# Kernel optimization log

Measured on AMD Instinct MI355X. Metric: run time of the kernel, lower is better.

Reference implementation:

```python
import jax, jax.numpy as jnp
import numpy as np

B, S, C, H, L = 8, 1000, 512, 8, 6
D = C // H  # 64


def setup_inputs() -> dict:
    key = jax.random.key(0)
    ks = jax.random.split(key, 6)
    s = 0.02
    x = jax.random.normal(ks[0], (B, S, C), dtype=jnp.float32)
    ln_g = jnp.ones((L, C), jnp.float32)
    ln_b = jnp.zeros((L, C), jnp.float32)
    Wq = jax.random.normal(ks[1], (L, C, C), jnp.float32) * s
    Wk = jax.random.normal(ks[2], (L, C, C), jnp.float32) * s
    Wv = jax.random.normal(ks[3], (L, C, C), jnp.float32) * s
    Wo = jax.random.normal(ks[4], (L, C, C), jnp.float32) * s
    bq = jnp.zeros((L, C), jnp.float32)
    bk = jnp.zeros((L, C), jnp.float32)
    bv = jnp.zeros((L, C), jnp.float32)
    bo = jnp.zeros((L, C), jnp.float32)
    return dict(x=x, ln_g=ln_g, ln_b=ln_b, Wq=Wq, bq=bq, Wk=Wk, bk=bk,
                Wv=Wv, bv=bv, Wo=Wo, bo=bo)


def _layer_norm(x, g, b, eps=1e-5):
    m = jnp.mean(x, axis=-1, keepdims=True)
    v = jnp.mean(jnp.square(x - m), axis=-1, keepdims=True)
    return (x - m) * jax.lax.rsqrt(v + eps) * g + b


def reference(x, ln_g, ln_b, Wq, bq, Wk, bk, Wv, bv, Wo, bo):
    # First streaming call: history is empty, so q = k = v = x for every
    # layer (x is never updated between layers); only the last layer's
    # output is returned. Mask is all-ones (no-op); dropout is eval-mode.
    Bn, Sn, Cn = x.shape
    scale = 1.0 / np.sqrt(D).astype(np.float32)
    # additive relative-position bias: pos[i, j] = i - j
    pos = (jnp.arange(Sn)[:, None] - jnp.arange(Sn)[None, :]).astype(x.dtype)
    out = x
    for i in range(L):
        xn = _layer_norm(x, ln_g[i], ln_b[i])  # same LN for q, k, v
        q = (xn @ Wq[i].T + bq[i]).reshape(Bn, Sn, H, D)
        k = (xn @ Wk[i].T + bk[i]).reshape(Bn, Sn, H, D)
        v = (xn @ Wv[i].T + bv[i]).reshape(Bn, Sn, H, D)
        scores = jnp.einsum('bqhd,bkhd->bhqk', q, k) * scale + pos  # [B,H,S,S]
        attn = jax.nn.softmax(scores, axis=-1)
        ctx = jnp.einsum('bhqk,bkhd->bqhd', attn, v).reshape(Bn, Sn, Cn)
        out = ctx @ Wo[i].T + bo[i]
    return out
```

## Files before the change

### kernel.cpp

```cpp
#include <hip/hip_runtime.h>
#include <math.h>


typedef __bf16 bf16x8 __attribute__((ext_vector_type(8)));
typedef __bf16 bf16x4 __attribute__((ext_vector_type(4)));
typedef float f32x4 __attribute__((ext_vector_type(4)));

__device__ __forceinline__ void async16(const __bf16* g, __bf16* l) {
  __builtin_amdgcn_global_load_lds((const __attribute__((address_space(1))) void*)g,
                                   (__attribute__((address_space(3))) void*)l, 16, 0, 0);
}

__global__ __launch_bounds__(256) void prep_k(const float* __restrict__ Wq, const float* __restrict__ Wk,
                                              const float* __restrict__ Wv, const float* __restrict__ Wo,
                                              __bf16* __restrict__ wdst,
                                              const float* __restrict__ x, const float* __restrict__ lg,
                                              const float* __restrict__ lb, __bf16* __restrict__ y) {
  const int bid = blockIdx.x;
  if (bid < 1024) {
    const float* src = (bid < 256) ? Wq : (bid < 512) ? Wk : (bid < 768) ? Wv : Wo;
    int idx = ((bid & 255) * 256 + threadIdx.x) * 4;
    float4 v = *(const float4*)(src + idx);
    bf16x4 o = {(__bf16)v.x, (__bf16)v.y, (__bf16)v.z, (__bf16)v.w};
    *(bf16x4*)(wdst + (size_t)(bid >> 8) * 262144 + idx) = o;
    return;
  }
  const int row = (bid - 1024) * 4 + (threadIdx.x >> 6);
  const int l = threadIdx.x & 63;
  const float* xr = x + (size_t)row * 512 + l * 8;
  float4 a = *(const float4*)xr, c = *(const float4*)(xr + 4);
  float s = a.x + a.y + a.z + a.w + c.x + c.y + c.z + c.w;
#pragma unroll
  for (int m = 1; m < 64; m <<= 1) s += __shfl_xor(s, m, 64);
  float mean = s * (1.0f / 512.0f);
  float d[8] = {a.x - mean, a.y - mean, a.z - mean, a.w - mean,
                c.x - mean, c.y - mean, c.z - mean, c.w - mean};
  float qq = 0.f;
#pragma unroll
  for (int e = 0; e < 8; ++e) qq += d[e] * d[e];
#pragma unroll
  for (int m = 1; m < 64; m <<= 1) qq += __shfl_xor(qq, m, 64);
  float rstd = rsqrtf(qq * (1.0f / 512.0f) + 1e-5f);
  float4 g0 = *(const float4*)(lg + l * 8), g1 = *(const float4*)(lg + l * 8 + 4);
  float4 b0 = *(const float4*)(lb + l * 8), b1 = *(const float4*)(lb + l * 8 + 4);
  float gg[8] = {g0.x, g0.y, g0.z, g0.w, g1.x, g1.y, g1.z, g1.w};
  float bb[8] = {b0.x, b0.y, b0.z, b0.w, b1.x, b1.y, b1.z, b1.w};
  bf16x8 o;
#pragma unroll
  for (int e = 0; e < 8; ++e) o[e] = (__bf16)(d[e] * rstd * gg[e] + bb[e]);
  *(bf16x8*)(y + (size_t)row * 512 + l * 8) = o;
}

template <int PROJ>
__global__ __launch_bounds__(256) void gemm_k(const __bf16* __restrict__ A,
                                              const __bf16* __restrict__ Wq_,
                                              const __bf16* __restrict__ Wkv_,
                                              const float* __restrict__ bq_,
                                              const float* __restrict__ bk_,
                                              const float* __restrict__ bv_,
                                              void* __restrict__ Yq_,
                                              __bf16* __restrict__ Ykv_,
                                              int idbase) {
  __shared__ __align__(16) __bf16 Ws[64 * 512];
  const int t = threadIdx.x, w = t >> 6, l = t & 63, g = l >> 4, l15 = l & 15;
  const int id = blockIdx.x + idbase;

  const __bf16* Ab;
  const __bf16* Wt;
  const float* bp;
  int maxrow, ldY;
  void* Yp;
  if (PROJ || id < 512) {
    int low3 = id & 7, rest = id >> 3;
    int n = rest & 7, m = (rest >> 3) * 8 + low3;
    if (m >= 63) return;
    Ab = A + (size_t)m * 128 * 512;
    maxrow = 8000 - m * 128; if (maxrow > 128) maxrow = 128;
    Wt = Wq_ + (size_t)n * 64 * 512;
    bp = bq_ + n * 64;
    ldY = 512;
    Yp = (float*)Yq_ + (size_t)m * 128 * 512 + n * 64;
  } else {
    int kid = id - 512;
    int b = kid & 7, n = kid >> 3;
    Ab = A + (size_t)b * 1000 * 512;
    maxrow = 128;
    Wt = Wkv_ + (size_t)n * 64 * 512;
    int nc = n * 64;
    bp = (nc < 512) ? (bk_ + nc) : (bv_ + (nc - 512));
    ldY = 1024;
    Yp = Ykv_ + (size_t)b * 128 * 1024 + nc;
  }

  float bias_j[4];
#pragma unroll
  for (int j = 0; j < 4; ++j) bias_j[j] = bp[j * 16 + l15];

  int r0 = w * 32 + l15, r1 = r0 + 16;
  int cr0 = (r0 < maxrow) ? r0 : (maxrow - 1);
  int cr1 = (r1 < maxrow) ? r1 : (maxrow - 1);
  const __bf16* a0p = Ab + (size_t)cr0 * 512 + g * 8;
  const __bf16* a1p = Ab + (size_t)cr1 * 512 + g * 8;
  bf16x8 a0 = *(const bf16x8*)a0p;
  bf16x8 a1 = *(const bf16x8*)a1p;

#pragma unroll
  for (int i = 0; i < 16; ++i) {
    int s = i * 256 + t;
    int row = s >> 6, u = s & 63;
    async16(Wt + (size_t)row * 512 + ((u ^ (row & 7)) << 3), &Ws[s * 8]);
  }
  __syncthreads();

  f32x4 acc[2][4] = {};
#pragma unroll
  for (int ks = 0; ks < 16; ++ks) {
    bf16x8 ca0 = a0, ca1 = a1;
    if (ks < 15) {
      a0 = *(const bf16x8*)(a0p + (ks + 1) * 32);
      a1 = *(const bf16x8*)(a1p + (ks + 1) * 32);
    }
    bf16x8 bfr[4];
#pragma unroll
    for (int j = 0; j < 4; ++j) {
      int rb = j * 16 + l15;
      int u = ks * 4 + g;
      bfr[j] = *(const bf16x8*)&Ws[rb * 512 + ((u ^ (rb & 7)) << 3)];
    }
#pragma unroll
    for (int j = 0; j < 4; ++j) {
      acc[0][j] = __builtin_amdgcn_mfma_f32_16x16x32_bf16(ca0, bfr[j], acc[0][j], 0, 0, 0);
      acc[1][j] = __builtin_amdgcn_mfma_f32_16x16x32_bf16(ca1, bfr[j], acc[1][j], 0, 0, 0);
    }
  }

#pragma unroll
  for (int strip = 0; strip < 2; ++strip)
#pragma unroll
    for (int r = 0; r < 4; ++r) {
      int lrow = w * 32 + strip * 16 + g * 4 + r;
      if (lrow < maxrow) {
#pragma unroll
        for (int j = 0; j < 4; ++j) {
          float val = acc[strip][j][r] + bias_j[j];
          if (PROJ) ((float*)Yp)[(size_t)lrow * ldY + j * 16 + l15] = val;
          else      ((__bf16*)Yp)[(size_t)lrow * ldY + j * 16 + l15] = (__bf16)val;
        }
      }
    }
}

__global__ __launch_bounds__(256) void attn_k(const __bf16* __restrict__ xn,
                                              const __bf16* __restrict__ wq,
                                              const float* __restrict__ bq,
                                              const __bf16* __restrict__ kv,
                                              __bf16* __restrict__ ctx) {
  __shared__ __align__(16) __bf16 arena[32768];
  __bf16* Ks = arena;
  __bf16* Vt = arena + 8192;
  __bf16* Qs = arena + 16384;
  __bf16* Ps = arena + 20480;
  const int t = threadIdx.x, w = t >> 6, l = t & 63, g = l >> 4, l15 = l & 15;
  const int id = blockIdx.x;
  const int h = id >> 7, b = (id >> 4) & 7, q0 = (id & 15) * 64;

  const __bf16* Wt = wq + (size_t)h * 64 * 512;
#pragma unroll
  for (int i = 0; i < 16; ++i) {
    int s = i * 256 + t;
    int row = s >> 6, u = s & 63;
    async16(Wt + (size_t)row * 512 + ((u ^ (row & 7)) << 3), &arena[s * 8]);
  }
  int qr = q0 + w * 16 + l15;
  int cqr = (qr > 999) ? 999 : qr;
  const __bf16* a0p = xn + ((size_t)(b * 1000 + cqr)) * 512 + g * 8;
  bf16x8 a0 = *(const bf16x8*)a0p;
  float bias_j[4];
#pragma unroll
  for (int j = 0; j < 4; ++j) bias_j[j] = bq[h * 64 + j * 16 + l15];
  __syncthreads();

  f32x4 acc[4] = {};
#pragma unroll
  for (int ks = 0; ks < 16; ++ks) {
    bf16x8 ca = a0;
    if (ks < 15) a0 = *(const bf16x8*)(a0p + (ks + 1) * 32);
    bf16x8 bfr[4];
#pragma unroll
    for (int j = 0; j < 4; ++j) {
      int rb = j * 16 + l15;
      int u = ks * 4 + g;
      bfr[j] = *(const bf16x8*)&arena[rb * 512 + ((u ^ (rb & 7)) << 3)];
    }
#pragma unroll
    for (int j = 0; j < 4; ++j)
      acc[j] = __builtin_amdgcn_mfma_f32_16x16x32_bf16(ca, bfr[j], acc[j], 0, 0, 0);
  }
  __syncthreads();

#pragma unroll
  for (int i = 0; i < 4; ++i) {
    int s = i * 256 + t;
    int row = s >> 3, u = s & 7;
    async16(kv + (size_t)(b * 128 + row) * 1024 + h * 64 + ((u ^ (row & 7)) << 3), &Ks[s * 8]);
  }
  {
    int vrow = t & 127, dbase = (t >> 7) * 32;
    const __bf16* vp = kv + (size_t)(b * 128 + vrow) * 1024 + 512 + h * 64 + dbase;
#pragma unroll
    for (int c = 0; c < 4; ++c) {
      bf16x8 vv = *(const bf16x8*)(vp + c * 8);
#pragma unroll
      for (int e = 0; e < 8; ++e) {
        int d = dbase + c * 8 + e;
        Vt[d * 128 + (((vrow >> 3) ^ (d & 7)) << 3) + (vrow & 7)] = vv[e];
      }
    }
  }
#pragma unroll
  for (int j = 0; j < 4; ++j)
#pragma unroll
    for (int r = 0; r < 4; ++r) {
      int row = w * 16 + g * 4 + r, col = j * 16 + l15;
      Qs[row * 64 + ((((col >> 3) ^ (row & 7))) << 3) + (col & 7)] =
          (__bf16)(acc[j][r] + bias_j[j]);
    }
  bf16x8 aq[2];
  {
    int row = w * 16 + l15;
    aq[0] = *(const bf16x8*)&Qs[row * 64 + ((g ^ (row & 7)) << 3)];
    aq[1] = *(const bf16x8*)&Qs[row * 64 + (((4 + g) ^ (row & 7)) << 3)];
  }
  __syncthreads();

  f32x4 ct[8] = {};
#pragma unroll
  for (int c = 0; c < 2; ++c)
#pragma unroll
    for (int nt = 0; nt < 8; ++nt) {
      int rn = nt * 16 + l15;
      bf16x8 bkf = *(const bf16x8*)&Ks[rn * 64 + (((c * 4 + g) ^ (rn & 7)) << 3)];
      ct[nt] = __builtin_amdgcn_mfma_f32_16x16x32_bf16(aq[c], bkf, ct[nt], 0, 0, 0);
    }

  __bf16* Pw = Ps + w * 2176;
  float rs[4] = {0.f, 0.f, 0.f, 0.f};
#pragma unroll
  for (int nt = 0; nt < 8; ++nt) {
    int kg = nt * 16 + l15;
#pragma unroll
    for (int r = 0; r < 4; ++r) {
      float p = __expf(ct[nt][r] * 0.125f - (float)kg - 2.0f);
      __bf16 pb = (__bf16)p;
      Pw[(g * 4 + r) * 136 + kg] = pb;
      rs[r] += (float)pb;
    }
  }
#pragma unroll
  for (int r = 0; r < 4; ++r) {
    float s = rs[r];
    s += __shfl_xor(s, 1, 16);
    s += __shfl_xor(s, 2, 16);
    s += __shfl_xor(s, 4, 16);
    s += __shfl_xor(s, 8, 16);
    rs[r] = 1.0f / s;
  }

  f32x4 co[4] = {};
  bf16x8 ap[4];
#pragma unroll
  for (int c = 0; c < 4; ++c) ap[c] = *(const bf16x8*)&Pw[l15 * 136 + c * 32 + g * 8];
#pragma unroll
  for (int nt = 0; nt < 4; ++nt) {
    int d = nt * 16 + l15;
#pragma unroll
    for (int c = 0; c < 4; ++c) {
      bf16x8 bv = *(const bf16x8*)&Vt[d * 128 + (((c * 4 + g) ^ (d & 7)) << 3)];
      co[nt] = __builtin_amdgcn_mfma_f32_16x16x32_bf16(ap[c], bv, co[nt], 0, 0, 0);
    }
  }

#pragma unroll
  for (int r = 0; r < 4; ++r) {
    int qg = q0 + w * 16 + g * 4 + r;
    if (qg < 1000) {
      __bf16* op = ctx + ((size_t)(b * 1000 + qg)) * 512 + h * 64 + l15;
#pragma unroll
      for (int nt = 0; nt < 4; ++nt) op[nt * 16] = (__bf16)(co[nt][r] * rs[r]);
    }
  }
}

extern "C" void kernel_launch(void* const* d_in, const int* in_sizes, int n_in,
                              void* d_out, int out_size, void* d_ws, size_t ws_size,
                              hipStream_t stream) {
  const float* x    = (const float*)d_in[0];
  const float* ln_g = (const float*)d_in[1];
  const float* ln_b = (const float*)d_in[2];
  const float* Wq   = (const float*)d_in[3];
  const float* bq   = (const float*)d_in[4];
  const float* Wk   = (const float*)d_in[5];
  const float* bk   = (const float*)d_in[6];
  const float* Wv   = (const float*)d_in[7];
  const float* bv   = (const float*)d_in[8];
  const float* Wo   = (const float*)d_in[9];
  const float* bo   = (const float*)d_in[10];
  float* out = (float*)d_out;
  __bf16* ws = (__bf16*)d_ws;

  __bf16* xn  = ws;
  __bf16* ctx = ws + 4096000;
  __bf16* kvb = ws + 8192000;
  __bf16* wqb = ws + 9240576;
  __bf16* wkv = wqb + 262144;
  __bf16* wob = wqb + 786432;

  const size_t LW = (size_t)5 * 512 * 512;
  const size_t LB = (size_t)5 * 512;

  prep_k<<<3024, 256, 0, stream>>>(Wq + LW, Wk + LW, Wv + LW, Wo + LW, wqb,
                                   x, ln_g + LB, ln_b + LB, xn);
  gemm_k<0><<<128, 256, 0, stream>>>(xn, nullptr, wkv, nullptr, bk + LB, bv + LB,
                                     nullptr, kvb, 512);
  attn_k<<<1024, 256, 0, stream>>>(xn, wqb, bq + LB, kvb, ctx);
  gemm_k<1><<<512, 256, 0, stream>>>(ctx, wob, nullptr, bo + LB, nullptr, nullptr,
                                     out, nullptr, 0);
}
```

Before: 139.6 us.

## Fuse KV projection into prep kernel with inline layernorm and weight conversion

Merges the prep kernel and the K/V projection GEMM into one launch. KV blocks now convert fp32 Wk/Wv to bf16 directly into shared memory and compute layernorm stats on the fly from raw x, instead of reading pre-normalized xn. This removes one kernel launch and the serial dependency on prep, at the cost of redundant x reads and a one-pass variance formula. The output-projection GEMM is split into its own specialized kernel.

Result: slower. 145.5 us (+4.3%).

```diff
diff --git a/kernel.cpp b/kernel.cpp
--- a/kernel.cpp
+++ b/kernel.cpp
@@ -11,115 +11,127 @@
                                    (__attribute__((address_space(3))) void*)l, 16, 0, 0);
 }
 
-__global__ __launch_bounds__(256) void prep_k(const float* __restrict__ Wq, const float* __restrict__ Wk,
-                                              const float* __restrict__ Wv, const float* __restrict__ Wo,
-                                              __bf16* __restrict__ wdst,
-                                              const float* __restrict__ x, const float* __restrict__ lg,
-                                              const float* __restrict__ lb, __bf16* __restrict__ y) {
-  const int bid = blockIdx.x;
-  if (bid < 1024) {
-    const float* src = (bid < 256) ? Wq : (bid < 512) ? Wk : (bid < 768) ? Wv : Wo;
-    int idx = ((bid & 255) * 256 + threadIdx.x) * 4;
-    float4 v = *(const float4*)(src + idx);
-    bf16x4 o = {(__bf16)v.x, (__bf16)v.y, (__bf16)v.z, (__bf16)v.w};
-    *(bf16x4*)(wdst + (size_t)(bid >> 8) * 262144 + idx) = o;
+__device__ __forceinline__ bf16x8 norm8(float4 a, float4 c, float4 ga, float4 gc,
+                                        float4 ba, float4 bc, float m, float r) {
+  bf16x8 o;
+  o[0] = (__bf16)((a.x - m) * r * ga.x + ba.x);
+  o[1] = (__bf16)((a.y - m) * r * ga.y + ba.y);
+  o[2] = (__bf16)((a.z - m) * r * ga.z + ba.z);
+  o[3] = (__bf16)((a.w - m) * r * ga.w + ba.w);
+  o[4] = (__bf16)((c.x - m) * r * gc.x + bc.x);
+  o[5] = (__bf16)((c.y - m) * r * gc.y + bc.y);
+  o[6] = (__bf16)((c.z - m) * r * gc.z + bc.z);
+  o[7] = (__bf16)((c.w - m) * r * gc.w + bc.w);
+  return o;
+}
+
+__global__ __launch_bounds__(256) void prep_kv_k(
+    const float* __restrict__ x, const float* __restrict__ lg,
+    const float* __restrict__ lb,
+    const float* __restrict__ Wq, const float* __restrict__ Wo,
+    const float* __restrict__ Wk, const float* __restrict__ Wv,
+    const float* __restrict__ bk, const float* __restrict__ bv,
+    __bf16* __restrict__ wqb, __bf16* __restrict__ wob,
+    __bf16* __restrict__ xn, __bf16* __restrict__ Ykv) {
+  __shared__ __align__(16) __bf16 Ws[64 * 512];
+  const int t = threadIdx.x;
+  const int id = blockIdx.x;
+
+  if (id >= 128) {
+    int u = id - 128;
+    if (u < 512) {
+      const float* src = (u < 256) ? Wq : Wo;
+      __bf16* dst = (u < 256) ? wqb : wob;
+      int idx = ((u & 255) * 256 + t) * 4;
+      float4 v = *(const float4*)(src + idx);
+      bf16x4 o = {(__bf16)v.x, (__bf16)v.y, (__bf16)v.z, (__bf16)v.w};
+      *(bf16x4*)(dst + idx) = o;
+      return;
+    }
+    const int row = (u - 512) * 4 + (t >> 6);
+    const int l = t & 63;
+    const float* xr = x + (size_t)row * 512 + l * 8;
+    float4 a = *(const float4*)xr, c = *(const float4*)(xr + 4);
+    float s = a.x + a.y + a.z + a.w + c.x + c.y + c.z + c.w;
+#pragma unroll
+    for (int m = 1; m < 64; m <<= 1) s += __shfl_xor(s, m, 64);
+    float mean = s * (1.0f / 512.0f);
+    float d[8] = {a.x - mean, a.y - mean, a.z - mean, a.w - mean,
+                  c.x - mean, c.y - mean, c.z - mean, c.w - mean};
+    float qq = 0.f;
+#pragma unroll
+    for (int e = 0; e < 8; ++e) qq += d[e] * d[e];
+#pragma unroll
+    for (int m = 1; m < 64; m <<= 1) qq += __shfl_xor(qq, m, 64);
+    float rstd = rsqrtf(qq * (1.0f / 512.0f) + 1e-5f);
+    float4 g0 = *(const float4*)(lg + l * 8), g1 = *(const float4*)(lg + l * 8 + 4);
+    float4 b0 = *(const float4*)(lb + l * 8), b1 = *(const float4*)(lb + l * 8 + 4);
+    float gg[8] = {g0.x, g0.y, g0.z, g0.w, g1.x, g1.y, g1.z, g1.w};
+    float bb[8] = {b0.x, b0.y, b0.z, b0.w, b1.x, b1.y, b1.z, b1.w};
+    bf16x8 o;
+#pragma unroll
+    for (int e = 0; e < 8; ++e) o[e] = (__bf16)(d[e] * rstd * gg[e] + bb[e]);
+    *(bf16x8*)(xn + (size_t)row * 512 + l * 8) = o;
     return;
   }
-  const int row = (bid - 1024) * 4 + (threadIdx.x >> 6);
-  const int l = threadIdx.x & 63;
-  const float* xr = x + (size_t)row * 512 + l * 8;
-  float4 a = *(const float4*)xr, c = *(const float4*)(xr + 4);
-  float s = a.x + a.y + a.z + a.w + c.x + c.y + c.z + c.w;
-#pragma unroll
-  for (int m = 1; m < 64; m <<= 1) s += __shfl_xor(s, m, 64);
-  float mean = s * (1.0f / 512.0f);
-  float d[8] = {a.x - mean, a.y - mean, a.z - mean, a.w - mean,
-                c.x - mean, c.y - mean, c.z - mean, c.w - mean};
-  float qq = 0.f;
-#pragma unroll
-  for (int e = 0; e < 8; ++e) qq += d[e] * d[e];
-#pragma unroll
-  for (int m = 1; m < 64; m <<= 1) qq += __shfl_xor(qq, m, 64);
-  float rstd = rsqrtf(qq * (1.0f / 512.0f) + 1e-5f);
-  float4 g0 = *(const float4*)(lg + l * 8), g1 = *(const float4*)(lg + l * 8 + 4);
-  float4 b0 = *(const float4*)(lb + l * 8), b1 = *(const float4*)(lb + l * 8 + 4);
-  float gg[8] = {g0.x, g0.y, g0.z, g0.w, g1.x, g1.y, g1.z, g1.w};
-  float bb[8] = {b0.x, b0.y, b0.z, b0.w, b1.x, b1.y, b1.z, b1.w};
-  bf16x8 o;
-#pragma unroll
-  for (int e = 0; e < 8; ++e) o[e] = (__bf16)(d[e] * rstd * gg[e] + bb[e]);
-  *(bf16x8*)(y + (size_t)row * 512 + l * 8) = o;
-}
-
-template <int PROJ>
-__global__ __launch_bounds__(256) void gemm_k(const __bf16* __restrict__ A,
-                                              const __bf16* __restrict__ Wq_,
-                                              const __bf16* __restrict__ Wkv_,
-                                              const float* __restrict__ bq_,
-                                              const float* __restrict__ bk_,
-                                              const float* __restrict__ bv_,
-                                              void* __restrict__ Yq_,
-                                              __bf16* __restrict__ Ykv_,
-                                              int idbase) {
-  __shared__ __align__(16) __bf16 Ws[64 * 512];
-  const int t = threadIdx.x, w = t >> 6, l = t & 63, g = l >> 4, l15 = l & 15;
-  const int id = blockIdx.x + idbase;
-
-  const __bf16* Ab;
-  const __bf16* Wt;
-  const float* bp;
-  int maxrow, ldY;
-  void* Yp;
-  if (PROJ || id < 512) {
-    int low3 = id & 7, rest = id >> 3;
-    int n = rest & 7, m = (rest >> 3) * 8 + low3;
-    if (m >= 63) return;
-    Ab = A + (size_t)m * 128 * 512;
-    maxrow = 8000 - m * 128; if (maxrow > 128) maxrow = 128;
-    Wt = Wq_ + (size_t)n * 64 * 512;
-    bp = bq_ + n * 64;
-    ldY = 512;
-    Yp = (float*)Yq_ + (size_t)m * 128 * 512 + n * 64;
-  } else {
-    int kid = id - 512;
-    int b = kid & 7, n = kid >> 3;
-    Ab = A + (size_t)b * 1000 * 512;
-    maxrow = 128;
-    Wt = Wkv_ + (size_t)n * 64 * 512;
-    int nc = n * 64;
-    bp = (nc < 512) ? (bk_ + nc) : (bv_ + (nc - 512));
-    ldY = 1024;
-    Yp = Ykv_ + (size_t)b * 128 * 1024 + nc;
-  }
-
-  float bias_j[4];
-#pragma unroll
-  for (int j = 0; j < 4; ++j) bias_j[j] = bp[j * 16 + l15];
-
-  int r0 = w * 32 + l15, r1 = r0 + 16;
-  int cr0 = (r0 < maxrow) ? r0 : (maxrow - 1);
-  int cr1 = (r1 < maxrow) ? r1 : (maxrow - 1);
-  const __bf16* a0p = Ab + (size_t)cr0 * 512 + g * 8;
-  const __bf16* a1p = Ab + (size_t)cr1 * 512 + g * 8;
-  bf16x8 a0 = *(const bf16x8*)a0p;
-  bf16x8 a1 = *(const bf16x8*)a1p;
+
+  const int w = t >> 6, l = t & 63, g = l >> 4, l15 = l & 15;
+  const int b = id & 7, n = id >> 3;
+  const float* Wsrc = (n < 8) ? (Wk + (size_t)n * 64 * 512)
+                              : (Wv + (size_t)(n - 8) * 64 * 512);
+  const float* bp = (n < 8) ? (bk + n * 64) : (bv + (n - 8) * 64);
 
 #pragma unroll
   for (int i = 0; i < 16; ++i) {
     int s = i * 256 + t;
     int row = s >> 6, u = s & 63;
-    async16(Wt + (size_t)row * 512 + ((u ^ (row & 7)) << 3), &Ws[s * 8]);
-  }
+    const float* gp = Wsrc + (size_t)row * 512 + ((u ^ (row & 7)) << 3);
+    float4 f0 = *(const float4*)gp, f1 = *(const float4*)(gp + 4);
+    bf16x8 o = {(__bf16)f0.x, (__bf16)f0.y, (__bf16)f0.z, (__bf16)f0.w,
+                (__bf16)f1.x, (__bf16)f1.y, (__bf16)f1.z, (__bf16)f1.w};
+    *(bf16x8*)&Ws[s * 8] = o;
+  }
+
+  const int r0 = w * 32 + l15, r1 = r0 + 16;
+  const float* x0 = x + (size_t)(b * 1000 + r0) * 512;
+  const float* x1 = x + (size_t)(b * 1000 + r1) * 512;
+  float s0 = 0.f, q0 = 0.f, s1 = 0.f, q1 = 0.f;
+#pragma unroll
+  for (int ks = 0; ks < 16; ++ks) {
+    int off = ks * 32 + g * 8;
+    float4 a = *(const float4*)(x0 + off), c = *(const float4*)(x0 + off + 4);
+    float4 d = *(const float4*)(x1 + off), e = *(const float4*)(x1 + off + 4);
+    s0 += a.x + a.y + a.z + a.w + c.x + c.y + c.z + c.w;
+    q0 += a.x * a.x + a.y * a.y + a.z * a.z + a.w * a.w +
+          c.x * c.x + c.y * c.y + c.z * c.z + c.w * c.w;
+    s1 += d.x + d.y + d.z + d.w + e.x + e.y + e.z + e.w;
+    q1 += d.x * d.x + d.y * d.y + d.z * d.z + d.w * d.w +
+          e.x * e.x + e.y * e.y + e.z * e.z + e.w * e.w;
+  }
+  s0 += __shfl_xor(s0, 16, 64); q0 += __shfl_xor(q0, 16, 64);
+  s1 += __shfl_xor(s1, 16, 64); q1 += __shfl_xor(q1, 16, 64);
+  s0 += __shfl_xor(s0, 32, 64); q0 += __shfl_xor(q0, 32, 64);
+  s1 += __shfl_xor(s1, 32, 64); q1 += __shfl_xor(q1, 32, 64);
+  const float m0 = s0 * (1.f / 512.f), m1 = s1 * (1.f / 512.f);
+  const float rst0 = rsqrtf(fmaxf(q0 * (1.f / 512.f) - m0 * m0, 0.f) + 1e-5f);
+  const float rst1 = rsqrtf(fmaxf(q1 * (1.f / 512.f) - m1 * m1, 0.f) + 1e-5f);
+
+  float bias_j[4];
+#pragma unroll
+  for (int j = 0; j < 4; ++j) bias_j[j] = bp[j * 16 + l15];
+
   __syncthreads();
 
   f32x4 acc[2][4] = {};
-#pragma unroll
+#pragma unroll 2
   for (int ks = 0; ks < 16; ++ks) {
-    bf16x8 ca0 = a0, ca1 = a1;
-    if (ks < 15) {
-      a0 = *(const bf16x8*)(a0p + (ks + 1) * 32);
-      a1 = *(const bf16x8*)(a1p + (ks + 1) * 32);
-    }
+    int off = ks * 32 + g * 8;
+    float4 ga = *(const float4*)(lg + off), gc = *(const float4*)(lg + off + 4);
+    float4 ba = *(const float4*)(lb + off), bc = *(const float4*)(lb + off + 4);
+    float4 a = *(const float4*)(x0 + off), c = *(const float4*)(x0 + off + 4);
+    float4 d = *(const float4*)(x1 + off), e = *(const float4*)(x1 + off + 4);
+    bf16x8 ca0 = norm8(a, c, ga, gc, ba, bc, m0, rst0);
+    bf16x8 ca1 = norm8(d, e, ga, gc, ba, bc, m1, rst1);
     bf16x8 bfr[4];
 #pragma unroll
     for (int j = 0; j < 4; ++j) {
@@ -134,19 +146,15 @@
     }
   }
 
+  __bf16* Yp = Ykv + (size_t)b * 128 * 1024 + n * 64;
 #pragma unroll
   for (int strip = 0; strip < 2; ++strip)
 #pragma unroll
     for (int r = 0; r < 4; ++r) {
       int lrow = w * 32 + strip * 16 + g * 4 + r;
-      if (lrow < maxrow) {
-#pragma unroll
-        for (int j = 0; j < 4; ++j) {
-          float val = acc[strip][j][r] + bias_j[j];
-          if (PROJ) ((float*)Yp)[(size_t)lrow * ldY + j * 16 + l15] = val;
-          else      ((__bf16*)Yp)[(size_t)lrow * ldY + j * 16 + l15] = (__bf16)val;
-        }
-      }
+#pragma unroll
+      for (int j = 0; j < 4; ++j)
+        Yp[(size_t)lrow * 1024 + j * 16 + l15] = (__bf16)(acc[strip][j][r] + bias_j[j]);
     }
 }
 
@@ -291,20 +299,93 @@
   }
 }
 
+__global__ __launch_bounds__(256) void outproj_k(const __bf16* __restrict__ A,
+                                                 const __bf16* __restrict__ Wo_,
+                                                 const float* __restrict__ bo_,
+                                                 float* __restrict__ Y) {
+  __shared__ __align__(16) __bf16 Ws[64 * 512];
+  const int t = threadIdx.x, w = t >> 6, l = t & 63, g = l >> 4, l15 = l & 15;
+  const int id = blockIdx.x;
+  int low3 = id & 7, rest = id >> 3;
+  int n = rest & 7, m = (rest >> 3) * 8 + low3;
+  if (m >= 63) return;
+  const __bf16* Ab = A + (size_t)m * 128 * 512;
+  int maxrow = 8000 - m * 128; if (maxrow > 128) maxrow = 128;
+  const __bf16* Wt = Wo_ + (size_t)n * 64 * 512;
+  float* Yp = Y + (size_t)m * 128 * 512 + n * 64;
+
+  float bias_j[4];
+#pragma unroll
+  for (int j = 0; j < 4; ++j) bias_j[j] = bo_[n * 64 + j * 16 + l15];
+
+  int r0 = w * 32 + l15, r1 = r0 + 16;
+  int cr0 = (r0 < maxrow) ? r0 : (maxrow - 1);
+  int cr1 = (r1 < maxrow) ? r1 : (maxrow - 1);
+  const __bf16* a0p = Ab + (size_t)cr0 * 512 + g * 8;
+  const __bf16* a1p = Ab + (size_t)cr1 * 512 + g * 8;
+  bf16x8 a0 = *(const bf16x8*)a0p;
+  bf16x8 a1 = *(const bf16x8*)a1p;
+
+#pragma unroll
+  for (int i = 0; i < 16; ++i) {
+    int s = i * 256 + t;
+    int row = s >> 6, u = s & 63;
+    async16(Wt + (size_t)row * 512 + ((u ^ (row & 7)) << 3), &Ws[s * 8]);
+  }
+  __syncthreads();
+
+  f32x4 acc[2][4] = {};
+#pragma unroll
+  for (int ks = 0; ks < 16; ++ks) {
+    bf16x8 ca0 = a0, ca1 = a1;
+    if (ks < 15) {
+      a0 = *(const bf16x8*)(a0p + (ks + 1) * 32);
+      a1 = *(const bf16x8*)(a1p + (ks + 1) * 32);
+    }
+    bf16x8 bfr[4];
+#pragma unroll
+    for (int j = 0; j < 4; ++j) {
+      int rb = j * 16 + l15;
+      int u = ks * 4 + g;
+      bfr[j] = *(const bf16x8*)&Ws[rb * 512 + ((u ^ (rb & 7)) << 3)];
+    }
+#pragma unroll
+    for (int j = 0; j < 4; ++j) {
+      acc[0][j] = __builtin_amdgcn_mfma_f32_16x16x32_bf16(ca0, bfr[j], acc[0][j], 0, 0, 0);
+      acc[1][j] = __builtin_amdgcn_mfma_f32_16x16x32_bf16(ca1, bfr[j], acc[1][j], 0, 0, 0);
+    }
+  }
+
+#pragma unroll
+  for (int strip = 0; strip < 2; ++strip)
+#pragma unroll
+    for (int r = 0; r < 4; ++r) {
+      int lrow = w * 32 + strip * 16 + g * 4 + r;
+      if (lrow < maxrow) {
+#pragma unroll
+        for (int j = 0; j < 4; ++j)
+          Yp[(size_t)lrow * 512 + j * 16 + l15] = acc[strip][j][r] + bias_j[j];
+      }
+    }
+}
+
 extern "C" void kernel_launch(void* const* d_in, const int* in_sizes, int n_in,
                               void* d_out, int out_size, void* d_ws, size_t ws_size,
                               hipStream_t stream) {
-  const float* x    = (const float*)d_in[0];
-  const float* ln_g = (const float*)d_in[1];
-  const float* ln_b = (const float*)d_in[2];
-  const float* Wq   = (const float*)d_in[3];
-  const float* bq   = (const float*)d_in[4];
-  const float* Wk   = (const float*)d_in[5];
-  const float* bk   = (const float*)d_in[6];
-  const float* Wv   = (const float*)d_in[7];
-  const float* bv   = (const float*)d_in[8];
-  const float* Wo   = (const float*)d_in[9];
-  const float* bo   = (const float*)d_in[10];
+  const size_t LW = (size_t)5 * 512 * 512;
+  const size_t LB = (size_t)5 * 512;
+
+  const float* x   = (const float*)d_in[0];
+  const float* lg5 = (const float*)d_in[1] + LB;
+  const float* lb5 = (const float*)d_in[2] + LB;
+  const float* Wq5 = (const float*)d_in[3] + LW;
+  const float* bq5 = (const float*)d_in[4] + LB;
+  const float* Wk5 = (const float*)d_in[5] + LW;
+  const float* bk5 = (const float*)d_in[6] + LB;
+  const float* Wv5 = (const float*)d_in[7] + LW;
+  const float* bv5 = (const float*)d_in[8] + LB;
+  const float* Wo5 = (const float*)d_in[9] + LW;
+  const float* bo5 = (const float*)d_in[10] + LB;
   float* out = (float*)d_out;
   __bf16* ws = (__bf16*)d_ws;
 
@@ -312,17 +393,10 @@
   __bf16* ctx = ws + 4096000;
   __bf16* kvb = ws + 8192000;
   __bf16* wqb = ws + 9240576;
-  __bf16* wkv = wqb + 262144;
   __bf16* wob = wqb + 786432;
 
-  const size_t LW = (size_t)5 * 512 * 512;
-  const size_t LB = (size_t)5 * 512;
-
-  prep_k<<<3024, 256, 0, stream>>>(Wq + LW, Wk + LW, Wv + LW, Wo + LW, wqb,
-                                   x, ln_g + LB, ln_b + LB, xn);
-  gemm_k<0><<<128, 256, 0, stream>>>(xn, nullptr, wkv, nullptr, bk + LB, bv + LB,
-                                     nullptr, kvb, 512);
-  attn_k<<<1024, 256, 0, stream>>>(xn, wqb, bq + LB, kvb, ctx);
-  gemm_k<1><<<512, 256, 0, stream>>>(ctx, wob, nullptr, bo + LB, nullptr, nullptr,
-                                     out, nullptr, 0);
-}
+  prep_kv_k<<<2640, 256, 0, stream>>>(x, lg5, lb5, Wq5, Wo5, Wk5, Wv5, bk5, bv5,
+                                      wqb, wob, xn, kvb);
+  attn_k<<<1024, 256, 0, stream>>>(xn, wqb, bq5, kvb, ctx);
+  outproj_k<<<512, 256, 0, stream>>>(ctx, wob, bo5, out);
+}
```
